# Kernel tuning notes

Hardware: AMD Instinct MI355X
Metric: run time of the kernel (lower is better)

Reference implementation:

```python
import jax, jax.numpy as jnp
import numpy as np

D = 128        # dim_features
I = 3          # num_iterations (forward uses I+1 slices)
P = 64         # num_projections
Q = 100        # num_quantiles
G = 1000       # number of graphs in the batch
N = 200000     # total nodes
POW = 2        # p of the p-sliced Wasserstein


def setup_inputs() -> dict:
    key = jax.random.key(0)
    k1, k2, k3 = jax.random.split(key, 3)
    x = jax.random.normal(k1, (N, (I + 1) * D), dtype=jnp.float32)
    batch = jnp.sort(jax.random.randint(k2, (N,), 0, G, dtype=jnp.int32))
    proj = jax.random.normal(k3, (D, P), dtype=jnp.float32)
    proj = proj / jnp.sqrt(jnp.sum(proj ** 2, axis=0, keepdims=True))
    cum_weights = jnp.linspace(0.0, 1.0, Q, dtype=jnp.float32)
    return {"x": x, "batch": batch, "projections": proj, "cum_weights": cum_weights}


def reference(x, batch, projections, cum_weights):
    n = x.shape[0]
    # project all WL iterations at once: [N, I+1, D] @ [D, P] -> [N, I+1, P]
    xp = jnp.einsum('nid,dp->nip', x.reshape(n, I + 1, D), projections)

    # segment bookkeeping (batch is sorted, segments contiguous)
    counts = jax.ops.segment_sum(jnp.ones((n,), jnp.int32), batch, num_segments=G)
    starts = jnp.cumsum(counts) - counts  # exclusive prefix sum
    # torch.quantile(..., interpolation='lower'): index = floor(q * (len-1))
    qidx = starts[:, None] + jnp.floor(
        cum_weights[None, :] * jnp.maximum(counts - 1, 0)[:, None].astype(cum_weights.dtype)
    ).astype(jnp.int32)  # [G, Q]

    # segmented sort: per column, lexsort by (batch primary, value secondary)
    def sort_col(v):  # v: [N]
        order = jnp.lexsort((v, batch))
        return v[order]

    flat = xp.reshape(n, (I + 1) * P)
    sorted_vals = jax.vmap(sort_col, in_axes=1, out_axes=1)(flat)  # [N, (I+1)*P]

    quant = sorted_vals[qidx]                       # [G, Q, (I+1)*P]
    quant = quant.reshape(G, Q, I + 1, P)
    quant = jnp.transpose(quant, (0, 2, 1, 3))       # [G, I+1, Q, P] (torch flattens [Q,P] Q-major, concat over i)
    scale = (Q * P) ** (1.0 / POW)
    return (quant / scale).reshape(G, (I + 1) * Q * P)
```

## Files before the change

### kernel.cpp

```cpp
#include <hip/hip_runtime.h>
#include <cstdint>
#include <cstddef>

#define NN 200000
#define DD 128
#define II 4
#define PP 64
#define QQ 100
#define GG 1000

__global__ void starts_kernel(const int* __restrict__ batch, int* __restrict__ starts) {
    int g = blockIdx.x * blockDim.x + threadIdx.x;
    if (g > GG) return;
    if (g == GG) { starts[g] = NN; return; }
    int lo = 0, hi = NN;
    while (lo < hi) {
        int mid = (lo + hi) >> 1;
        if (batch[mid] < g) lo = mid + 1; else hi = mid;
    }
    starts[g] = lo;
}

__global__ __launch_bounds__(256) void proj_kernel(
        const float* __restrict__ x, const float* __restrict__ proj,
        float* __restrict__ xp_i, int i) {
    __shared__ float xs[64 * 129];
    const int t    = threadIdx.x;
    const int n0   = blockIdx.x * 64;
    const int lane = t & 63;
    const int pg   = __builtin_amdgcn_readfirstlane(t >> 6);

    {
        const int c4 = t & 31;
        const int r0 = t >> 5;
        #pragma unroll
        for (int pass = 0; pass < 8; ++pass) {
            const int row = r0 + pass * 8;
            const float4 v = *(const float4*)(x + (size_t)(n0 + row) * 512 + i * 128 + c4 * 4);
            float* dst = xs + row * 129 + c4 * 4;
            dst[0] = v.x; dst[1] = v.y; dst[2] = v.z; dst[3] = v.w;
        }
    }
    __syncthreads();

    float acc[16];
    #pragma unroll
    for (int pp = 0; pp < 16; ++pp) acc[pp] = 0.f;

    const float* __restrict__ pbase = proj + pg * 16;
    const float* __restrict__ xrow  = xs + lane * 129;
    #pragma unroll 4
    for (int d = 0; d < 128; ++d) {
        const float xv = xrow[d];
        #pragma unroll
        for (int pp = 0; pp < 16; ++pp)
            acc[pp] += xv * pbase[d * 64 + pp];
    }

    #pragma unroll
    for (int pp = 0; pp < 16; ++pp)
        xp_i[(size_t)(pg * 16 + pp) * NN + n0 + lane] = acc[pp];
}

template<int VPT>
__device__ inline void bitonic_sort(float v[VPT], int lane) {
    constexpr int NS = VPT * 64;
    #pragma unroll
    for (int k = 2; k <= NS; k <<= 1) {
        #pragma unroll
        for (int j = k >> 1; j >= 1; j >>= 1) {
            if (j >= VPT) {
                const int  d        = j / VPT;
                const bool up       = ((lane * VPT) & k) == 0;
                const bool lower    = (lane & d) == 0;
                const bool keep_min = (up == lower);
                #pragma unroll
                for (int r = 0; r < VPT; ++r) {
                    const float pv = __shfl_xor(v[r], d);
                    const float mn = fminf(v[r], pv);
                    const float mx = fmaxf(v[r], pv);
                    v[r] = keep_min ? mn : mx;
                }
            } else {
                #pragma unroll
                for (int r = 0; r < VPT; ++r) {
                    if ((r & j) == 0) {
                        const int  r2 = r | j;
                        const bool up = (((lane * VPT + r) & k) == 0);
                        const float a = v[r], b = v[r2];
                        const float mn = fminf(a, b), mx = fmaxf(a, b);
                        v[r]  = up ? mn : mx;
                        v[r2] = up ? mx : mn;
                    }
                }
            }
        }
    }
}

__global__ __launch_bounds__(1024) void sort_quant_kernel(
        const float* __restrict__ xp_i, const int* __restrict__ starts,
        const float* __restrict__ cw, float* __restrict__ out, int i) {
    __shared__ float sbuf[16 * 513];
    const int b    = blockIdx.x;
    const int g    = b >> 2;
    const int pq   = b & 3;
    const int t    = threadIdx.x;
    const int w    = __builtin_amdgcn_readfirstlane(t >> 6);
    const int lane = t & 63;

    const int start = starts[g];
    const int cnt   = starts[g + 1] - start;

    const int col = pq * 16 + w;
    const float* __restrict__ src = xp_i + (size_t)col * NN + start;
    float* lrow = sbuf + w * 513;

    if (cnt <= 256) {
        float v[4];
        #pragma unroll
        for (int r = 0; r < 4; ++r) {
            const int e = lane * 4 + r;
            v[r] = (e < cnt) ? src[e] : __builtin_inff();
        }
        bitonic_sort<4>(v, lane);
        #pragma unroll
        for (int r = 0; r < 4; ++r) lrow[lane * 4 + r] = v[r];
    } else {
        float v[8];
        #pragma unroll
        for (int r = 0; r < 8; ++r) {
            const int e = lane * 8 + r;
            v[r] = (e < cnt && e < 512) ? src[e] : __builtin_inff();
        }
        bitonic_sort<8>(v, lane);
        #pragma unroll
        for (int r = 0; r < 8; ++r) lrow[lane * 8 + r] = v[r];
    }
    __syncthreads();

    const float cm1 = (float)(cnt > 0 ? cnt - 1 : 0);
    const int   pl  = t & 15;
    const int   qt  = t >> 4;
    const float inv_scale = 1.0f / 80.0f;
    float* __restrict__ orow = out + (size_t)g * 25600 + i * 6400 + pq * 16 + pl;

    {
        const int q  = qt;
        int tq = (int)floorf(cw[q] * cm1);
        if (tq > 511) tq = 511;
        orow[q * 64] = sbuf[pl * 513 + tq] * inv_scale;
    }
    if (qt < QQ - 64) {
        const int q  = 64 + qt;
        int tq = (int)floorf(cw[q] * cm1);
        if (tq > 511) tq = 511;
        orow[q * 64] = sbuf[pl * 513 + tq] * inv_scale;
    }
}

extern "C" void kernel_launch(void* const* d_in, const int* in_sizes, int n_in,
                              void* d_out, int out_size, void* d_ws, size_t ws_size,
                              hipStream_t stream) {
    const float* x     = (const float*)d_in[0];
    const int*   batch = (const int*)  d_in[1];
    const float* proj  = (const float*)d_in[2];
    const float* cw    = (const float*)d_in[3];
    float*       out   = (float*)d_out;

    int*   starts = (int*)d_ws;
    float* xp_i   = (float*)((char*)d_ws + 4096);

    starts_kernel<<<4, 256, 0, stream>>>(batch, starts);

    for (int i = 0; i < II; ++i) {
        proj_kernel<<<NN / 64, 256, 0, stream>>>(x, proj, xp_i, i);
        sort_quant_kernel<<<GG * 4, 1024, 0, stream>>>(xp_i, starts, cw, out, i);
    }
}
```

Measured before the change: 963.8 us.

## Batch all iterations into single 2D-grid launches and shrink sort blocks

Replaces the per-iteration loop of eight kernel launches with one projection launch and one sort launch, each using blockIdx.y for the WL iteration, and writes the full projected tensor for all iterations to workspace. The shared-memory tile is padded to 132 so rows can be stored and read as float4, vectorizing LDS traffic in the projection inner loop. Sort blocks shrink from 1024 to 512 threads (8 columns per block) to improve occupancy and scheduling granularity. The change needs four times the workspace for the projected data, and the 132-float row stride may introduce LDS bank conflicts.

Measured after the change: 894.7 us. -7.2%, faster.

```diff
diff --git a/kernel.cpp b/kernel.cpp
--- a/kernel.cpp
+++ b/kernel.cpp
@@ -23,10 +23,11 @@
 
 __global__ __launch_bounds__(256) void proj_kernel(
         const float* __restrict__ x, const float* __restrict__ proj,
-        float* __restrict__ xp_i, int i) {
-    __shared__ float xs[64 * 129];
+        float* __restrict__ xp) {
+    __shared__ float xs[64 * 132];
     const int t    = threadIdx.x;
     const int n0   = blockIdx.x * 64;
+    const int i    = blockIdx.y;
     const int lane = t & 63;
     const int pg   = __builtin_amdgcn_readfirstlane(t >> 6);
 
@@ -37,8 +38,7 @@
         for (int pass = 0; pass < 8; ++pass) {
             const int row = r0 + pass * 8;
             const float4 v = *(const float4*)(x + (size_t)(n0 + row) * 512 + i * 128 + c4 * 4);
-            float* dst = xs + row * 129 + c4 * 4;
-            dst[0] = v.x; dst[1] = v.y; dst[2] = v.z; dst[3] = v.w;
+            *(float4*)(xs + row * 132 + c4 * 4) = v;
         }
     }
     __syncthreads();
@@ -48,18 +48,25 @@
     for (int pp = 0; pp < 16; ++pp) acc[pp] = 0.f;
 
     const float* __restrict__ pbase = proj + pg * 16;
-    const float* __restrict__ xrow  = xs + lane * 129;
+    const float* __restrict__ xrow  = xs + lane * 132;
+
     #pragma unroll 4
-    for (int d = 0; d < 128; ++d) {
-        const float xv = xrow[d];
+    for (int d4 = 0; d4 < 32; ++d4) {
+        const float4 xv = *(const float4*)(xrow + d4 * 4);
         #pragma unroll
-        for (int pp = 0; pp < 16; ++pp)
-            acc[pp] += xv * pbase[d * 64 + pp];
+        for (int pp = 0; pp < 16; ++pp) acc[pp] += xv.x * pbase[(d4 * 4 + 0) * 64 + pp];
+        #pragma unroll
+        for (int pp = 0; pp < 16; ++pp) acc[pp] += xv.y * pbase[(d4 * 4 + 1) * 64 + pp];
+        #pragma unroll
+        for (int pp = 0; pp < 16; ++pp) acc[pp] += xv.z * pbase[(d4 * 4 + 2) * 64 + pp];
+        #pragma unroll
+        for (int pp = 0; pp < 16; ++pp) acc[pp] += xv.w * pbase[(d4 * 4 + 3) * 64 + pp];
     }
 
+    float* __restrict__ obase = xp + ((size_t)i * 64 + pg * 16) * NN + n0 + lane;
     #pragma unroll
     for (int pp = 0; pp < 16; ++pp)
-        xp_i[(size_t)(pg * 16 + pp) * NN + n0 + lane] = acc[pp];
+        obase[(size_t)pp * NN] = acc[pp];
 }
 
 template<int VPT>
@@ -98,13 +105,14 @@
     }
 }
 
-__global__ __launch_bounds__(1024) void sort_quant_kernel(
-        const float* __restrict__ xp_i, const int* __restrict__ starts,
-        const float* __restrict__ cw, float* __restrict__ out, int i) {
-    __shared__ float sbuf[16 * 513];
+__global__ __launch_bounds__(512) void sort_quant_kernel(
+        const float* __restrict__ xp, const int* __restrict__ starts,
+        const float* __restrict__ cw, float* __restrict__ out) {
+    __shared__ float sbuf[8 * 513];
     const int b    = blockIdx.x;
-    const int g    = b >> 2;
-    const int pq   = b & 3;
+    const int g    = b >> 3;
+    const int pq   = b & 7;
+    const int i    = blockIdx.y;
     const int t    = threadIdx.x;
     const int w    = __builtin_amdgcn_readfirstlane(t >> 6);
     const int lane = t & 63;
@@ -112,8 +120,8 @@
     const int start = starts[g];
     const int cnt   = starts[g + 1] - start;
 
-    const int col = pq * 16 + w;
-    const float* __restrict__ src = xp_i + (size_t)col * NN + start;
+    const int col = pq * 8 + w;
+    const float* __restrict__ src = xp + ((size_t)i * 64 + col) * NN + start;
     float* lrow = sbuf + w * 513;
 
     if (cnt <= 256) {
@@ -140,10 +148,10 @@
     __syncthreads();
 
     const float cm1 = (float)(cnt > 0 ? cnt - 1 : 0);
-    const int   pl  = t & 15;
-    const int   qt  = t >> 4;
+    const int   pl  = t & 7;
+    const int   qt  = t >> 3;
     const float inv_scale = 1.0f / 80.0f;
-    float* __restrict__ orow = out + (size_t)g * 25600 + i * 6400 + pq * 16 + pl;
+    float* __restrict__ orow = out + (size_t)g * 25600 + i * 6400 + pq * 8 + pl;
 
     {
         const int q  = qt;
@@ -169,12 +177,9 @@
     float*       out   = (float*)d_out;
 
     int*   starts = (int*)d_ws;
-    float* xp_i   = (float*)((char*)d_ws + 4096);
+    float* xp     = (float*)((char*)d_ws + 4096);
 
     starts_kernel<<<4, 256, 0, stream>>>(batch, starts);
-
-    for (int i = 0; i < II; ++i) {
-        proj_kernel<<<NN / 64, 256, 0, stream>>>(x, proj, xp_i, i);
-        sort_quant_kernel<<<GG * 4, 1024, 0, stream>>>(xp_i, starts, cw, out, i);
-    }
+    proj_kernel<<<dim3(NN / 64, II), 256, 0, stream>>>(x, proj, xp);
+    sort_quant_kernel<<<dim3(GG * 8, II), 512, 0, stream>>>(xp, starts, cw, out);
 }
```
